# Kernel tuning notes

Measured on AMD Instinct MI355X. Metric: run time of the kernel, lower is better.

Reference implementation:

```python
import jax, jax.numpy as jnp
import numpy as np

DIM = 128
HEADS = 8
HD = DIM // HEADS          # 16
KS = 8                     # neighborhood kernel size
STRIDE = 2                 # GNA query-group stride
DIL = 2                    # dilation


def axis_indices(L, k, s, d):
    """Per-axis neighborhood indices [L, k] for dilated, strided, edge-clamped NA.

    Queries are grouped in blocks of `s`; every query in a block shares the
    window of the block's center query (GNA 'stride'). Dilation partitions the
    axis into `d` sub-grids; the window lives on the center query's sub-grid
    and is clamped so it never leaves the axis (natten-style sliding window).
    """
    idx = np.zeros((L, k), dtype=np.int32)
    for i in range(L):
        ic = min((i // s) * s + (s - 1) // 2, L - 1)   # group-center query
        r = ic % d                                      # sub-grid (residue)
        Lsub = (L - r + d - 1) // d                     # sub-grid length
        ii = ic // d                                    # index within sub-grid
        start = min(max(ii - (k - 1) // 2, 0), max(Lsub - k, 0))
        for j in range(k):
            idx[i, j] = r + d * min(start + j, Lsub - 1)
    return idx


def setup_inputs() -> dict:
    key = jax.random.key(0)
    ks = jax.random.split(key, 5)
    x = jax.random.normal(ks[0], (1, DIM, 96, 96), jnp.float32)
    # depthwise-grouped qkv conv: Conv2d(dim, 3*dim, 3, 1, 1, groups=dim)
    qkv_w = jax.random.normal(ks[1], (3 * DIM, 1, 3, 3), jnp.float32) * 0.1
    qkv_b = jax.random.normal(ks[2], (3 * DIM,), jnp.float32) * 0.02
    # 1x1 projection: Conv2d(dim, dim, 1)
    proj_w = jax.random.normal(ks[3], (DIM, DIM, 1, 1), jnp.float32) * (DIM ** -0.5)
    proj_b = jax.random.normal(ks[4], (DIM,), jnp.float32) * 0.02
    return {"x": x, "qkv_w": qkv_w, "qkv_b": qkv_b, "proj_w": proj_w, "proj_b": proj_b}


def reference(x, qkv_w, qkv_b, proj_w, proj_b):
    B, C, H, W = x.shape
    # grouped (groups=C) 3x3 conv producing q,k,v
    qkv = jax.lax.conv_general_dilated(
        x, qkv_w, window_strides=(1, 1), padding=[(1, 1), (1, 1)],
        dimension_numbers=("NCHW", "OIHW", "NCHW"), feature_group_count=C)
    qkv = qkv + qkv_b[None, :, None, None]
    qkv = qkv.reshape(B, 3, C, H, W)

    def to_heads(t):  # b c h w -> b h w nh hd
        return t.reshape(B, HEADS, HD, H, W).transpose(0, 3, 4, 1, 2)

    q = to_heads(qkv[:, 0])
    k = to_heads(qkv[:, 1])
    v = to_heads(qkv[:, 2])

    scale = HD ** -0.5
    ri = jnp.asarray(axis_indices(H, KS, STRIDE, DIL))  # [H, KS]
    ci = jnp.asarray(axis_indices(W, KS, STRIDE, DIL))  # [W, KS]
    R = ri[:, :, None, None]       # [H, KS, 1, 1]
    Cc = ci[None, None, :, :]      # [1, 1, W, KS]
    k_win = k[:, R, Cc]            # [B, H, KS, W, KS, nh, hd]
    v_win = v[:, R, Cc]

    logits = jnp.einsum("bijnd,bipjqnd->bijnpq", q * scale, k_win)
    attn = jax.nn.softmax(logits.reshape(B, H, W, HEADS, KS * KS), axis=-1)
    attn = attn.reshape(B, H, W, HEADS, KS, KS)
    out = jnp.einsum("bijnpq,bipjqnd->bijnd", attn, v_win)

    out = out.transpose(0, 3, 4, 1, 2).reshape(B, C, H, W)  # b h w nh hd -> b c h w
    out = jnp.einsum("bchw,oc->bohw", out, proj_w[:, :, 0, 0]) + proj_b[None, :, None, None]
    return out
```

## Files before the change

### kernel.cpp

```cpp
#include <hip/hip_runtime.h>
#include <hip/hip_bf16.h>

#define HH   96
#define WW   96
#define NPIX 9216
#define CH   128
#define NH   8
#define HD   16
#define KS   8

#define NEPIX   2304
#define QTP  136
#define KVTP 264
#define XP2  61
#define PP2  72

typedef __attribute__((ext_vector_type(8))) short bf16x8;
typedef __attribute__((ext_vector_type(4))) float f32x4;

__device__ __forceinline__ unsigned short f2bf(float f) {
    __hip_bfloat16 b = __float2bfloat16(f);
    union { __hip_bfloat16 b; unsigned short u; } cv; cv.b = b; return cv.u;
}
__device__ __forceinline__ bf16x8 u4_as_bf(uint4 u) {
    union { uint4 u; bf16x8 b; } cv; cv.u = u; return cv.b;
}

__global__ __launch_bounds__(256) void conv_kernel(
    const float* __restrict__ x,
    const float* __restrict__ w,
    const float* __restrict__ bias,
    unsigned short* __restrict__ q_pm,
    unsigned short* __restrict__ k_pm,
    unsigned short* __restrict__ vt_f)
{
    __shared__ float ldsx[128 * XP2];
    __shared__ unsigned short qt [12 * QTP];
    __shared__ unsigned short kvt[ 6 * KVTP];

    const int row = blockIdx.x >> 3;
    const int q8  = blockIdx.x & 7;
    const int j0q = q8 * 12;
    const int tid = threadIdx.x;
    const int g   = tid >> 1;
    const int sh  = tid & 1;
    const bool kvrow = (row & 1) == 0;

    #pragma unroll
    for (int it = 0; it < 8; ++it) {
        const int t = it * 256 + tid;
        if (t < 1920) {
            const int r   = t / 640;
            const int rem = t - r * 640;
            const int c   = rem / 5;
            const int s4  = rem - c * 5;
            const int rg  = row + r - 1;
            const int jj  = j0q - 4 + s4 * 4;
            float4 v = make_float4(0.f, 0.f, 0.f, 0.f);
            if (rg >= 0 && rg < HH && jj >= 0 && jj < WW)
                v = *(const float4*)(x + (size_t)c * NPIX + rg * WW + jj);
            *(float4*)&ldsx[c * XP2 + r * 20 + s4 * 4] = v;
        }
    }
    __syncthreads();

    float xr[3][8];
    {
        const float* xg_l = &ldsx[g * XP2 + 3 + sh * 6];
        #pragma unroll
        for (int dr = 0; dr < 3; ++dr)
            #pragma unroll
            for (int m = 0; m < 8; ++m)
                xr[dr][m] = xg_l[dr * 20 + m];
    }

    #pragma unroll
    for (int dt = 0; dt < 3; ++dt) {
        const int o = 3 * g + dt;
        const int t = o >> 7;
        const int c = o & 127;
        float w9[9];
        #pragma unroll
        for (int k = 0; k < 9; ++k) w9[k] = w[o * 9 + k];
        const float b = bias[o];

        if (t == 0) {
            #pragma unroll
            for (int px = 0; px < 6; ++px) {
                float acc = b;
                #pragma unroll
                for (int kh = 0; kh < 3; ++kh)
                    #pragma unroll
                    for (int kw = 0; kw < 3; ++kw)
                        acc += xr[kh][px + kw] * w9[kh * 3 + kw];
                qt[(sh * 6 + px) * QTP + c] = f2bf(acc);
            }
        } else if (kvrow) {
            #pragma unroll
            for (int pe = 0; pe < 3; ++pe) {
                const int px = pe * 2;
                float acc = b;
                #pragma unroll
                for (int kh = 0; kh < 3; ++kh)
                    #pragma unroll
                    for (int kw = 0; kw < 3; ++kw)
                        acc += xr[kh][px + kw] * w9[kh * 3 + kw];
                kvt[(sh * 3 + pe) * KVTP + (t - 1) * CH + c] = f2bf(acc);
            }
        }
    }

    __syncthreads();

    const int er = row >> 1;
    const int b6 = j0q >> 1;
    const int ntask = kvrow ? ((q8 == 0) ? 800 : 672) : 192;
    #pragma unroll
    for (int it = 0; it < 4; ++it) {
        const int idx = it * 256 + tid;
        if (idx < 192) {
            const int px = idx >> 4;
            const int c8 = (idx & 15) * 8;
            const uint4 v = *(const uint4*)&qt[px * QTP + c8];
            *(uint4*)(q_pm + ((size_t)(row * WW) + j0q + px) * CH + c8) = v;
        } else if (idx < 288 && kvrow) {
            const int k2  = idx - 192;
            const int epx = k2 >> 4;
            const int c8  = (k2 & 15) * 8;
            const uint4 v = *(const uint4*)&kvt[epx * KVTP + c8];
            *(uint4*)(k_pm + ((size_t)er * 48 + b6 + epx) * CH + c8) = v;
        } else if (idx < 672 && kvrow) {
            const int v2 = idx - 288;
            const int pr = v2 >> 7;
            const int c  = v2 & 127;
            const int colA  = b6 + pr * 2;
            const int chunk = colA >> 3;
            const int off   = colA & 7;
            const unsigned int a0 =
                (unsigned int)kvt[(pr * 2)     * KVTP + CH + c]
                | ((unsigned int)kvt[(pr * 2 + 1) * KVTP + CH + c] << 16);
            *(unsigned int*)(vt_f
                + (((size_t)(c >> 4) * 48 + er) * 7 + chunk) * 128
                + (c & 15) * 8 + off) = a0;
        } else if (idx < ntask) {
            const int zf = idx - 672;
            const int hh = zf >> 4;
            const int d  = zf & 15;
            *(uint4*)(vt_f + (((size_t)hh * 48 + er) * 7 + 6) * 128 + d * 8)
                = make_uint4(0u, 0u, 0u, 0u);
        }
    }
}

__global__ __launch_bounds__(512, 4) void attn_kernel(
    const unsigned short* __restrict__ q_pm,
    const unsigned short* __restrict__ k_pm,
    const unsigned short* __restrict__ vt_f,
    float* __restrict__ a_t)
{
    __shared__ unsigned short plds[NH][16 * PP2];

    const int seg = blockIdx.x;
    const int i   = seg / 6;
    const int j0  = (seg - i * 6) * 16;
    const int er0 = min(max(i / 2 - 3, 0), 40);
    const int ec0 = min(max(j0 / 2 - 3, 0), 40);
    const int ecs = ec0 >> 3;
    const int sh5 = ec0 & 7;

    const int tid  = threadIdx.x;
    const int h    = tid >> 6;
    const int lane = tid & 63;
    const int nn   = lane & 15;
    const int g    = lane >> 4;
    const int g4   = g * 4;

    const int j   = j0 + nn;
    const int ci0 = min(max(j / 2 - 3, 0), 40) - ec0;

    bf16x8 qf = (bf16x8)(short)0;
    if (g < 2)
        qf = u4_as_bf(*(const uint4*)(q_pm + (size_t)(seg * 16 + nn) * CH
                                      + h * HD + g * 8));
    const f32x4 zacc = {0.f, 0.f, 0.f, 0.f};
    f32x4 st[8];
    #pragma unroll
    for (int t = 0; t < 8; ++t) {
        bf16x8 kf = (bf16x8)(short)0;
        if (g < 2) {
            const int ep = (er0 + t) * 48 + min(ec0 + nn, 47);
            kf = u4_as_bf(*(const uint4*)(k_pm + (size_t)ep * CH
                                          + h * HD + g * 8));
        }
        st[t] = __builtin_amdgcn_mfma_f32_16x16x32_bf16(kf, qf, zacc, 0, 0, 0);
    }

    float m = -1e30f;
    #pragma unroll
    for (int t = 0; t < 8; ++t)
        #pragma unroll
        for (int r = 0; r < 4; ++r) {
            const int cc = g4 + r;
            float T = st[t][r] * 0.25f;
            T = ((unsigned)(cc - ci0) < 8u) ? T : -1e30f;
            st[t][r] = T;
            m = fmaxf(m, T);
        }
    m = fmaxf(m, __shfl_xor(m, 16));
    m = fmaxf(m, __shfl_xor(m, 32));

    float s = 0.f;
    #pragma unroll
    for (int t = 0; t < 8; ++t)
        #pragma unroll
        for (int r = 0; r < 4; ++r) {
            const float p = __expf(st[t][r] - m);
            st[t][r] = p;
            s += p;
        }
    s += __shfl_xor(s, 16);
    s += __shfl_xor(s, 32);

    unsigned short* pr = &plds[h][nn * PP2];
    f32x4 acc = {0.f, 0.f, 0.f, 0.f};

    #pragma unroll
    for (int hf = 0; hf < 2; ++hf) {
        #pragma unroll
        for (int tl = 0; tl < 4; ++tl) {
            const f32x4 P = st[hf * 4 + tl];
            const unsigned short a0 = f2bf(P[0]), a1 = f2bf(P[1]),
                                 a2 = f2bf(P[2]), a3 = f2bf(P[3]);
            *(uint2*)&pr[tl * 16 + g4] =
                make_uint2((unsigned)a0 | ((unsigned)a1 << 16),
                           (unsigned)a2 | ((unsigned)a3 << 16));
        }
        bf16x8 vfr[2];
        #pragma unroll
        for (int ks = 0; ks < 2; ++ks) {
            const int tl = ks * 2 + (g >> 1);
            const int er = er0 + hf * 4 + tl;
            const int ch = ecs + (g & 1);
            const unsigned short* vb = vt_f
                + ((size_t)(h * 48 + er) * 7 + ch) * 128 + nn * 8;
            const uint4 u0 = *(const uint4*)vb;
            if (sh5 == 0) {
                vfr[ks] = u4_as_bf(u0);
            } else {
                const uint4 u1 = *(const uint4*)(vb + 128);
                uint4 o;
                o.x = (u0.z >> 16) | (u0.w << 16);
                o.y = (u0.w >> 16) | (u1.x << 16);
                o.z = (u1.x >> 16) | (u1.y << 16);
                o.w = (u1.y >> 16) | (u1.z << 16);
                vfr[ks] = u4_as_bf(o);
            }
            const bf16x8 pb =
                u4_as_bf(*(const uint4*)&pr[tl * 16 + (g & 1) * 8]);
            acc = __builtin_amdgcn_mfma_f32_16x16x32_bf16(vfr[ks], pb, acc,
                                                          0, 0, 0);
        }
        __builtin_amdgcn_sched_barrier(0);
        #pragma unroll
        for (int tl = 0; tl < 4; ++tl) {
            const f32x4 P = st[hf * 4 + tl];
            unsigned short lo[4];
            #pragma unroll
            for (int r = 0; r < 4; ++r) {
                const unsigned short hi = f2bf(P[r]);
                lo[r] = f2bf(P[r] - __uint_as_float((unsigned)hi << 16));
            }
            *(uint2*)&pr[tl * 16 + g4] =
                make_uint2((unsigned)lo[0] | ((unsigned)lo[1] << 16),
                           (unsigned)lo[2] | ((unsigned)lo[3] << 16));
        }
        __builtin_amdgcn_sched_barrier(0);
        #pragma unroll
        for (int ks = 0; ks < 2; ++ks) {
            const int tl = ks * 2 + (g >> 1);
            const bf16x8 pb =
                u4_as_bf(*(const uint4*)&pr[tl * 16 + (g & 1) * 8]);
            acc = __builtin_amdgcn_mfma_f32_16x16x32_bf16(vfr[ks], pb, acc,
                                                          0, 0, 0);
        }
        __builtin_amdgcn_sched_barrier(0);
    }

    const float inv = 1.f / s;
    const int pix = seg * 16 + nn;
    #pragma unroll
    for (int r = 0; r < 4; ++r)
        a_t[(size_t)(h * HD + g4 + r) * NPIX + pix] = acc[r] * inv;
}

__global__ __launch_bounds__(256) void proj_kernel(
    const float* __restrict__ a_t,
    const float* __restrict__ pw,
    const float* __restrict__ pb,
    float* __restrict__ out)
{
    __shared__ float at[CH][36];

    const int tid = threadIdx.x;
    const int px0 = blockIdx.x * 32;

    #pragma unroll
    for (int it = 0; it < 4; ++it) {
        const int idx = it * 256 + tid;
        const int c   = idx >> 3;
        const int p4  = (idx & 7) * 4;
        *(float4*)&at[c][p4] =
            *(const float4*)(a_t + (size_t)c * NPIX + px0 + p4);
    }
    __syncthreads();

    const int og = tid >> 3;
    const int o0 = og * 4;
    const int p0 = (tid & 7) * 4;

    float acc[4][4];
    #pragma unroll
    for (int i = 0; i < 4; ++i) {
        const float b = pb[o0 + i];
        #pragma unroll
        for (int jj = 0; jj < 4; ++jj) acc[i][jj] = b;
    }

    #pragma unroll 2
    for (int c0 = 0; c0 < CH; c0 += 4) {
        float4 wv[4];
        #pragma unroll
        for (int i = 0; i < 4; ++i)
            wv[i] = *(const float4*)(pw + (size_t)(o0 + i) * CH + c0);
        float4 av[4];
        #pragma unroll
        for (int k = 0; k < 4; ++k)
            av[k] = *(const float4*)&at[c0 + k][p0];
        #pragma unroll
        for (int i = 0; i < 4; ++i) {
            acc[i][0] += wv[i].x * av[0].x; acc[i][1] += wv[i].x * av[0].y;
            acc[i][2] += wv[i].x * av[0].z; acc[i][3] += wv[i].x * av[0].w;
            acc[i][0] += wv[i].y * av[1].x; acc[i][1] += wv[i].y * av[1].y;
            acc[i][2] += wv[i].y * av[1].z; acc[i][3] += wv[i].y * av[1].w;
            acc[i][0] += wv[i].z * av[2].x; acc[i][1] += wv[i].z * av[2].y;
            acc[i][2] += wv[i].z * av[2].z; acc[i][3] += wv[i].z * av[2].w;
            acc[i][0] += wv[i].w * av[3].x; acc[i][1] += wv[i].w * av[3].y;
            acc[i][2] += wv[i].w * av[3].z; acc[i][3] += wv[i].w * av[3].w;
        }
    }

    #pragma unroll
    for (int i = 0; i < 4; ++i)
        *(float4*)(out + (size_t)(o0 + i) * NPIX + px0 + p0)
            = make_float4(acc[i][0], acc[i][1], acc[i][2], acc[i][3]);
}

extern "C" void kernel_launch(void* const* d_in, const int* in_sizes, int n_in,
                              void* d_out, int out_size, void* d_ws, size_t ws_size,
                              hipStream_t stream)
{
    const float* x      = (const float*)d_in[0];
    const float* qkv_w  = (const float*)d_in[1];
    const float* qkv_b  = (const float*)d_in[2];
    const float* proj_w = (const float*)d_in[3];
    const float* proj_b = (const float*)d_in[4];
    float* out = (float*)d_out;

    unsigned short* q_pm = (unsigned short*)d_ws;
    unsigned short* k_pm = q_pm + (size_t)NPIX * CH;
    unsigned short* vt_f = k_pm + (size_t)NEPIX * CH;
    float*          a_t  = (float*)(vt_f + (size_t)8 * 48 * 7 * 128);

    conv_kernel<<<768, 256, 0, stream>>>(x, qkv_w, qkv_b, q_pm, k_pm, vt_f);
    attn_kernel<<<576, 512, 0, stream>>>(q_pm, k_pm, vt_f, a_t);
    proj_kernel<<<288, 256, 0, stream>>>(a_t, proj_w, proj_b, out);
}
```

Measured before the change: 92.88 us.

## Use head-major Q/K layout, stage conv weights in LDS, split-bf16 P in one pass

Q and K are now stored head-major ([head][pixel][16]), so each attention wave reads a contiguous 32-byte-per-pixel block instead of strided 256-byte rows. The conv kernel loads its depthwise weights and biases into shared memory cooperatively rather than having each thread read them from global memory. In the attention kernel the hi and lo bf16 parts of P are written to separate halves of a wider LDS row. This lets the two P·V MFMAs per step issue back to back, with no second write phase and no scheduling barriers, at the cost of more LDS per block.

Result: no change. 92.98 us (+0.1%).

```diff
diff --git a/kernel.cpp b/kernel.cpp
--- a/kernel.cpp
+++ b/kernel.cpp
@@ -13,7 +13,7 @@
 #define QTP  136
 #define KVTP 264
 #define XP2  61
-#define PP2  72
+#define PP3  136
 
 typedef __attribute__((ext_vector_type(8))) short bf16x8;
 typedef __attribute__((ext_vector_type(4))) float f32x4;
@@ -35,6 +35,8 @@
     unsigned short* __restrict__ vt_f)
 {
     __shared__ float ldsx[128 * XP2];
+    __shared__ float wl[3456];
+    __shared__ float bl[384];
     __shared__ unsigned short qt [12 * QTP];
     __shared__ unsigned short kvt[ 6 * KVTP];
 
@@ -47,7 +49,7 @@
     const bool kvrow = (row & 1) == 0;
 
     #pragma unroll
-    for (int it = 0; it < 8; ++it) {
+    for (int it = 0; it < 12; ++it) {
         const int t = it * 256 + tid;
         if (t < 1920) {
             const int r   = t / 640;
@@ -60,6 +62,12 @@
             if (rg >= 0 && rg < HH && jj >= 0 && jj < WW)
                 v = *(const float4*)(x + (size_t)c * NPIX + rg * WW + jj);
             *(float4*)&ldsx[c * XP2 + r * 20 + s4 * 4] = v;
+        } else if (t < 2784) {
+            const int f = t - 1920;
+            *(float4*)&wl[f * 4] = *(const float4*)(w + f * 4);
+        } else if (t < 2880) {
+            const int f = t - 2784;
+            *(float4*)&bl[f * 4] = *(const float4*)(bias + f * 4);
         }
     }
     __syncthreads();
@@ -81,8 +89,8 @@
         const int c = o & 127;
         float w9[9];
         #pragma unroll
-        for (int k = 0; k < 9; ++k) w9[k] = w[o * 9 + k];
-        const float b = bias[o];
+        for (int k = 0; k < 9; ++k) w9[k] = wl[o * 9 + k];
+        const float b = bl[o];
 
         if (t == 0) {
             #pragma unroll
@@ -121,14 +129,20 @@
         if (idx < 192) {
             const int px = idx >> 4;
             const int c8 = (idx & 15) * 8;
+            const int hh = c8 >> 4;
+            const int d8 = c8 & 15;
             const uint4 v = *(const uint4*)&qt[px * QTP + c8];
-            *(uint4*)(q_pm + ((size_t)(row * WW) + j0q + px) * CH + c8) = v;
+            *(uint4*)(q_pm + ((size_t)hh * NPIX + row * WW + j0q + px) * 16
+                      + d8) = v;
         } else if (idx < 288 && kvrow) {
             const int k2  = idx - 192;
             const int epx = k2 >> 4;
             const int c8  = (k2 & 15) * 8;
+            const int hh  = c8 >> 4;
+            const int d8  = c8 & 15;
             const uint4 v = *(const uint4*)&kvt[epx * KVTP + c8];
-            *(uint4*)(k_pm + ((size_t)er * 48 + b6 + epx) * CH + c8) = v;
+            *(uint4*)(k_pm + ((size_t)hh * NEPIX + er * 48 + b6 + epx) * 16
+                      + d8) = v;
         } else if (idx < 672 && kvrow) {
             const int v2 = idx - 288;
             const int pr = v2 >> 7;
@@ -158,7 +172,7 @@
     const unsigned short* __restrict__ vt_f,
     float* __restrict__ a_t)
 {
-    __shared__ unsigned short plds[NH][16 * PP2];
+    __shared__ unsigned short plds[NH][16 * PP3];
 
     const int seg = blockIdx.x;
     const int i   = seg / 6;
@@ -180,8 +194,8 @@
 
     bf16x8 qf = (bf16x8)(short)0;
     if (g < 2)
-        qf = u4_as_bf(*(const uint4*)(q_pm + (size_t)(seg * 16 + nn) * CH
-                                      + h * HD + g * 8));
+        qf = u4_as_bf(*(const uint4*)(q_pm
+                + ((size_t)h * NPIX + seg * 16 + nn) * 16 + g * 8));
     const f32x4 zacc = {0.f, 0.f, 0.f, 0.f};
     f32x4 st[8];
     #pragma unroll
@@ -189,8 +203,8 @@
         bf16x8 kf = (bf16x8)(short)0;
         if (g < 2) {
             const int ep = (er0 + t) * 48 + min(ec0 + nn, 47);
-            kf = u4_as_bf(*(const uint4*)(k_pm + (size_t)ep * CH
-                                          + h * HD + g * 8));
+            kf = u4_as_bf(*(const uint4*)(k_pm
+                    + ((size_t)h * NEPIX + ep) * 16 + g * 8));
         }
         st[t] = __builtin_amdgcn_mfma_f32_16x16x32_bf16(kf, qf, zacc, 0, 0, 0);
     }
@@ -221,7 +235,7 @@
     s += __shfl_xor(s, 16);
     s += __shfl_xor(s, 32);
 
-    unsigned short* pr = &plds[h][nn * PP2];
+    unsigned short* pr = &plds[h][nn * PP3];
     f32x4 acc = {0.f, 0.f, 0.f, 0.f};
 
     #pragma unroll
@@ -229,13 +243,19 @@
         #pragma unroll
         for (int tl = 0; tl < 4; ++tl) {
             const f32x4 P = st[hf * 4 + tl];
-            const unsigned short a0 = f2bf(P[0]), a1 = f2bf(P[1]),
-                                 a2 = f2bf(P[2]), a3 = f2bf(P[3]);
+            unsigned short hi[4], lo[4];
+            #pragma unroll
+            for (int r = 0; r < 4; ++r) {
+                hi[r] = f2bf(P[r]);
+                lo[r] = f2bf(P[r] - __uint_as_float((unsigned)hi[r] << 16));
+            }
             *(uint2*)&pr[tl * 16 + g4] =
-                make_uint2((unsigned)a0 | ((unsigned)a1 << 16),
-                           (unsigned)a2 | ((unsigned)a3 << 16));
-        }
-        bf16x8 vfr[2];
+                make_uint2((unsigned)hi[0] | ((unsigned)hi[1] << 16),
+                           (unsigned)hi[2] | ((unsigned)hi[3] << 16));
+            *(uint2*)&pr[68 + tl * 16 + g4] =
+                make_uint2((unsigned)lo[0] | ((unsigned)lo[1] << 16),
+                           (unsigned)lo[2] | ((unsigned)lo[3] << 16));
+        }
         #pragma unroll
         for (int ks = 0; ks < 2; ++ks) {
             const int tl = ks * 2 + (g >> 1);
@@ -244,8 +264,9 @@
             const unsigned short* vb = vt_f
                 + ((size_t)(h * 48 + er) * 7 + ch) * 128 + nn * 8;
             const uint4 u0 = *(const uint4*)vb;
+            bf16x8 vf;
             if (sh5 == 0) {
-                vfr[ks] = u4_as_bf(u0);
+                vf = u4_as_bf(u0);
             } else {
                 const uint4 u1 = *(const uint4*)(vb + 128);
                 uint4 o;
@@ -253,37 +274,15 @@
                 o.y = (u0.w >> 16) | (u1.x << 16);
                 o.z = (u1.x >> 16) | (u1.y << 16);
                 o.w = (u1.y >> 16) | (u1.z << 16);
-                vfr[ks] = u4_as_bf(o);
+                vf = u4_as_bf(o);
             }
-            const bf16x8 pb =
+            const bf16x8 ph =
                 u4_as_bf(*(const uint4*)&pr[tl * 16 + (g & 1) * 8]);
-            acc = __builtin_amdgcn_mfma_f32_16x16x32_bf16(vfr[ks], pb, acc,
-                                                          0, 0, 0);
-        }
-        __builtin_amdgcn_sched_barrier(0);
-        #pragma unroll
-        for (int tl = 0; tl < 4; ++tl) {
-            const f32x4 P = st[hf * 4 + tl];
-            unsigned short lo[4];
-            #pragma unroll
-            for (int r = 0; r < 4; ++r) {
-                const unsigned short hi = f2bf(P[r]);
-                lo[r] = f2bf(P[r] - __uint_as_float((unsigned)hi << 16));
-            }
-            *(uint2*)&pr[tl * 16 + g4] =
-                make_uint2((unsigned)lo[0] | ((unsigned)lo[1] << 16),
-                           (unsigned)lo[2] | ((unsigned)lo[3] << 16));
-        }
-        __builtin_amdgcn_sched_barrier(0);
-        #pragma unroll
-        for (int ks = 0; ks < 2; ++ks) {
-            const int tl = ks * 2 + (g >> 1);
-            const bf16x8 pb =
-                u4_as_bf(*(const uint4*)&pr[tl * 16 + (g & 1) * 8]);
-            acc = __builtin_amdgcn_mfma_f32_16x16x32_bf16(vfr[ks], pb, acc,
-                                                          0, 0, 0);
-        }
-        __builtin_amdgcn_sched_barrier(0);
+            const bf16x8 po =
+                u4_as_bf(*(const uint4*)&pr[68 + tl * 16 + (g & 1) * 8]);
+            acc = __builtin_amdgcn_mfma_f32_16x16x32_bf16(vf, ph, acc, 0, 0, 0);
+            acc = __builtin_amdgcn_mfma_f32_16x16x32_bf16(vf, po, acc, 0, 0, 0);
+        }
     }
 
     const float inv = 1.f / s;
@@ -367,8 +366,8 @@
     float* out = (float*)d_out;
 
     unsigned short* q_pm = (unsigned short*)d_ws;
-    unsigned short* k_pm = q_pm + (size_t)NPIX * CH;
-    unsigned short* vt_f = k_pm + (size_t)NEPIX * CH;
+    unsigned short* k_pm = q_pm + (size_t)NH * NPIX * 16;
+    unsigned short* vt_f = k_pm + (size_t)NH * NEPIX * 16;
     float*          a_t  = (float*)(vt_f + (size_t)8 * 48 * 7 * 128);
 
     conv_kernel<<<768, 256, 0, stream>>>(x, qkv_w, qkv_b, q_pm, k_pm, vt_f);
```
